# Kernel optimization log

Measured on AMD Instinct MI355X. Metric: run time of the kernel, lower is better.

Reference implementation:

```python
import jax, jax.numpy as jnp
import numpy as np

B, L, Q, H = 8192, 200, 128, 128

def setup_inputs() -> dict:
    key = jax.random.key(0)
    k1, k2, k3, k4 = jax.random.split(key, 4)
    query_ad = jax.random.normal(k1, (B, Q), dtype=jnp.float32)
    hist_behavior = jax.random.normal(k2, (B, L, H), dtype=jnp.float32)
    hist_behavior_length = jax.random.randint(k3, (B,), 0, L, dtype=jnp.int64)
    # xavier_normal for [Q, H] weight: std = sqrt(2/(Q+H))
    std = float(np.sqrt(2.0 / (Q + H)))
    biInt_weight = jax.random.normal(k4, (Q, H), dtype=jnp.float32) * std
    return {
        "query_ad": query_ad,
        "hist_behavior": hist_behavior,
        "hist_behavior_length": hist_behavior_length,
        "biInt_weight": biInt_weight,
    }

def reference(query_ad, hist_behavior, hist_behavior_length, biInt_weight):
    # bilinear attention logits: [B, L]
    logits = jnp.einsum('bq,qh,blh->bl', query_ad, biInt_weight, hist_behavior)
    # faithful to original: mask fills positions where arange < length with 1e-9
    L_ = hist_behavior.shape[1]
    mask = jnp.arange(L_)[None, :] < hist_behavior_length[:, None]  # [B, L]
    logits = jnp.where(mask, jnp.float32(1e-9), logits)
    score = jax.nn.softmax(logits, axis=-1)  # [B, L]
    out = jnp.einsum('bl,blh->bh', score, hist_behavior)  # [B, H]
    return out
```

## Files before the change

kernel.cpp:

```cpp
#include <hip/hip_runtime.h>
#include <math.h>

#define L_SEQ 200
#define Q_DIM 128
#define H_DIM 128

__global__ __launch_bounds__(256, 3) void attn_pool(
    const float* __restrict__ query,
    const float* __restrict__ hist,
    const int*   __restrict__ lens,
    const float* __restrict__ W,
    float* __restrict__ out)
{
    const int b = blockIdx.x;
    const int t = threadIdx.x;
    const int lane32 = t & 31;
    const int lgroup = t >> 5;
    const int wid    = t >> 6;

    __shared__ float s_q[Q_DIM];
    __shared__ float s_qw[H_DIM];
    __shared__ float s_part[8 * H_DIM];
    __shared__ float s_logits[L_SEQ];
    __shared__ float s_red[4];
    __shared__ float s_scalar[2];

    if (t < Q_DIM) s_q[t] = query[(size_t)b * Q_DIM + t];
    __syncthreads();
    {
        const int h  = t & 127;
        const int qh = t >> 7;
        float acc = 0.f;
        #pragma unroll 8
        for (int i = 0; i < 64; ++i) {
            const int q = qh * 64 + i;
            acc = fmaf(s_q[q], W[q * H_DIM + h], acc);
        }
        s_part[t] = acc;
    }
    __syncthreads();
    if (t < H_DIM) s_qw[t] = s_part[t] + s_part[t + 128];
    __syncthreads();

    const float4 qw4 = reinterpret_cast<const float4*>(s_qw)[lane32];

    const float* hrow = hist + (size_t)b * (L_SEQ * H_DIM);
    float4 r[25];
    #pragma unroll
    for (int i = 0; i < 25; ++i) {
        const int l = i * 8 + lgroup;
        r[i] = reinterpret_cast<const float4*>(hrow + l * H_DIM)[lane32];
    }

    #pragma unroll
    for (int i = 0; i < 25; ++i) {
        float p = qw4.x * r[i].x + qw4.y * r[i].y + qw4.z * r[i].z + qw4.w * r[i].w;
        p += __shfl_down(p, 16, 32);
        p += __shfl_down(p, 8, 32);
        p += __shfl_down(p, 4, 32);
        p += __shfl_down(p, 2, 32);
        p += __shfl_down(p, 1, 32);
        if (lane32 == 0) s_logits[i * 8 + lgroup] = p;
    }
    __syncthreads();

    const int len = lens[b];
    float x = -3.0e38f;
    if (t < L_SEQ) {
        const float v = s_logits[t];
        x = (t < len) ? 1e-9f : v;
    }
    float m = x;
    m = fmaxf(m, __shfl_down(m, 32));
    m = fmaxf(m, __shfl_down(m, 16));
    m = fmaxf(m, __shfl_down(m, 8));
    m = fmaxf(m, __shfl_down(m, 4));
    m = fmaxf(m, __shfl_down(m, 2));
    m = fmaxf(m, __shfl_down(m, 1));
    if ((t & 63) == 0) s_red[wid] = m;
    __syncthreads();
    if (t == 0)
        s_scalar[0] = fmaxf(fmaxf(s_red[0], s_red[1]), fmaxf(s_red[2], s_red[3]));
    __syncthreads();
    const float gmax = s_scalar[0];

    float e = 0.f;
    if (t < L_SEQ) {
        e = __expf(x - gmax);
        s_logits[t] = e;
    }
    float ssum = e;
    ssum += __shfl_down(ssum, 32);
    ssum += __shfl_down(ssum, 16);
    ssum += __shfl_down(ssum, 8);
    ssum += __shfl_down(ssum, 4);
    ssum += __shfl_down(ssum, 2);
    ssum += __shfl_down(ssum, 1);
    if ((t & 63) == 0) s_red[wid] = ssum;
    __syncthreads();
    if (t == 0) s_scalar[1] = s_red[0] + s_red[1] + s_red[2] + s_red[3];
    __syncthreads();
    const float inv = 1.0f / s_scalar[1];

    float4 acc = make_float4(0.f, 0.f, 0.f, 0.f);
    #pragma unroll
    for (int i = 0; i < 25; ++i) {
        const float s = s_logits[i * 8 + lgroup] * inv;
        acc.x = fmaf(s, r[i].x, acc.x);
        acc.y = fmaf(s, r[i].y, acc.y);
        acc.z = fmaf(s, r[i].z, acc.z);
        acc.w = fmaf(s, r[i].w, acc.w);
    }
    reinterpret_cast<float4*>(s_part)[lgroup * 32 + lane32] = acc;
    __syncthreads();
    if (t < H_DIM) {
        float v = 0.f;
        #pragma unroll
        for (int g = 0; g < 8; ++g) v += s_part[g * H_DIM + t];
        out[(size_t)b * H_DIM + t] = v;
    }
}

extern "C" void kernel_launch(void* const* d_in, const int* in_sizes, int n_in,
                              void* d_out, int out_size, void* d_ws, size_t ws_size,
                              hipStream_t stream) {
    const float* query = (const float*)d_in[0];
    const float* hist  = (const float*)d_in[1];
    const int*   lens  = (const int*)d_in[2];
    const float* W     = (const float*)d_in[3];
    float* out = (float*)d_out;

    const int B = in_sizes[2];
    attn_pool<<<dim3(B), dim3(256), 0, stream>>>(query, hist, lens, W, out);
}
```

Before: 1.040 ms.

## Split query-weight GEMV into batched kernel and widen attention pooling blocks

Moves the per-row q·W product into a separate kernel that handles eight batch rows per block and reuses each W load across them, writing the result to workspace (or to the output buffer when workspace is too small). The attention kernel now runs 512 threads per block with 13 registers of float4 history per thread. It skips logit dot products for masked positions and replaces the block-level softmax reductions with per-wavefront shuffle reductions, recomputing the exponentials in the pooling loop. The cost is an extra launch and an extra round trip of qw through global memory.

```diff
diff --git a/kernel.cpp b/kernel.cpp
--- a/kernel.cpp
+++ b/kernel.cpp
@@ -4,119 +4,152 @@
 #define L_SEQ 200
 #define Q_DIM 128
 #define H_DIM 128
+#define QBATCH 8
 
-__global__ __launch_bounds__(256, 3) void attn_pool(
+__global__ __launch_bounds__(256, 4) void qw_gemv(
     const float* __restrict__ query,
-    const float* __restrict__ hist,
-    const int*   __restrict__ lens,
     const float* __restrict__ W,
-    float* __restrict__ out)
+    float* __restrict__ qw)
 {
-    const int b = blockIdx.x;
-    const int t = threadIdx.x;
-    const int lane32 = t & 31;
-    const int lgroup = t >> 5;
-    const int wid    = t >> 6;
+    const int t    = threadIdx.x;
+    const int h    = t & 127;
+    const int half = t >> 7;
+    const int b0   = blockIdx.x * QBATCH;
 
-    __shared__ float s_q[Q_DIM];
-    __shared__ float s_qw[H_DIM];
-    __shared__ float s_part[8 * H_DIM];
-    __shared__ float s_logits[L_SEQ];
-    __shared__ float s_red[4];
-    __shared__ float s_scalar[2];
+    __shared__ float s_q[QBATCH][Q_DIM];
+    __shared__ float s_acc[2][QBATCH][H_DIM];
 
-    if (t < Q_DIM) s_q[t] = query[(size_t)b * Q_DIM + t];
-    __syncthreads();
     {
-        const int h  = t & 127;
-        const int qh = t >> 7;
-        float acc = 0.f;
-        #pragma unroll 8
-        for (int i = 0; i < 64; ++i) {
-            const int q = qh * 64 + i;
-            acc = fmaf(s_q[q], W[q * H_DIM + h], acc);
-        }
-        s_part[t] = acc;
-    }
-    __syncthreads();
-    if (t < H_DIM) s_qw[t] = s_part[t] + s_part[t + 128];
-    __syncthreads();
-
-    const float4 qw4 = reinterpret_cast<const float4*>(s_qw)[lane32];
-
-    const float* hrow = hist + (size_t)b * (L_SEQ * H_DIM);
-    float4 r[25];
-    #pragma unroll
-    for (int i = 0; i < 25; ++i) {
-        const int l = i * 8 + lgroup;
-        r[i] = reinterpret_cast<const float4*>(hrow + l * H_DIM)[lane32];
-    }
-
-    #pragma unroll
-    for (int i = 0; i < 25; ++i) {
-        float p = qw4.x * r[i].x + qw4.y * r[i].y + qw4.z * r[i].z + qw4.w * r[i].w;
-        p += __shfl_down(p, 16, 32);
-        p += __shfl_down(p, 8, 32);
-        p += __shfl_down(p, 4, 32);
-        p += __shfl_down(p, 2, 32);
-        p += __shfl_down(p, 1, 32);
-        if (lane32 == 0) s_logits[i * 8 + lgroup] = p;
+        const int bb = t >> 5;
+        const int f4 = t & 31;
+        reinterpret_cast<float4*>(&s_q[bb][0])[f4] =
+            reinterpret_cast<const float4*>(query + (size_t)(b0 + bb) * Q_DIM)[f4];
     }
     __syncthreads();
 
+    float acc[QBATCH] = {};
+    const float* Wcol = W + half * 64 * H_DIM + h;
+    #pragma unroll 4
+    for (int i = 0; i < 64; ++i) {
+        const float wq = Wcol[i * H_DIM];
+        const int   q  = half * 64 + i;
+        #pragma unroll
+        for (int bb = 0; bb < QBATCH; ++bb)
+            acc[bb] = fmaf(s_q[bb][q], wq, acc[bb]);
+    }
+    #pragma unroll
+    for (int bb = 0; bb < QBATCH; ++bb) s_acc[half][bb][h] = acc[bb];
+    __syncthreads();
+
+    #pragma unroll
+    for (int k = 0; k < 4; ++k) {
+        const int idx = k * 256 + t;
+        const int bb  = idx >> 7;
+        const int hh  = idx & 127;
+        qw[(size_t)(b0 + bb) * H_DIM + hh] = s_acc[0][bb][hh] + s_acc[1][bb][hh];
+    }
+}
+
+__global__ __launch_bounds__(512, 4) void attn_pool(
+    const float* qw_all,
+    const float* __restrict__ hist,
+    const int*   __restrict__ lens,
+    float*       out)
+{
+    const int b      = blockIdx.x;
+    const int t      = threadIdx.x;
+    const int lane32 = t & 31;
+    const int lane64 = t & 63;
+    const int lgroup = t >> 5;
+
+    __shared__ float s_logits[L_SEQ];
+    __shared__ float s_part[16 * H_DIM];
+
+    const float4* hbase =
+        reinterpret_cast<const float4*>(hist + (size_t)b * (L_SEQ * H_DIM));
+    float4 r[13];
+    #pragma unroll
+    for (int i = 0; i < 13; ++i) {
+        const int l = i * 16 + lgroup;
+        if (i < 12 || lgroup < 8)
+            r[i] = hbase[l * 32 + lane32];
+    }
+
+    const float4 qw4 =
+        reinterpret_cast<const float4*>(qw_all + (size_t)b * H_DIM)[lane32];
     const int len = lens[b];
-    float x = -3.0e38f;
-    if (t < L_SEQ) {
-        const float v = s_logits[t];
-        x = (t < len) ? 1e-9f : v;
+
+    #pragma unroll
+    for (int i = 0; i < 13; ++i) {
+        const int l = i * 16 + lgroup;
+        if (i < 12 || lgroup < 8) {
+            if (l >= len) {
+                float p = qw4.x * r[i].x + qw4.y * r[i].y
+                        + qw4.z * r[i].z + qw4.w * r[i].w;
+                p += __shfl_down(p, 16, 32);
+                p += __shfl_down(p,  8, 32);
+                p += __shfl_down(p,  4, 32);
+                p += __shfl_down(p,  2, 32);
+                p += __shfl_down(p,  1, 32);
+                if (lane32 == 0) s_logits[l] = p;
+            }
+        }
     }
-    float m = x;
-    m = fmaxf(m, __shfl_down(m, 32));
-    m = fmaxf(m, __shfl_down(m, 16));
-    m = fmaxf(m, __shfl_down(m, 8));
-    m = fmaxf(m, __shfl_down(m, 4));
-    m = fmaxf(m, __shfl_down(m, 2));
-    m = fmaxf(m, __shfl_down(m, 1));
-    if ((t & 63) == 0) s_red[wid] = m;
     __syncthreads();
-    if (t == 0)
-        s_scalar[0] = fmaxf(fmaxf(s_red[0], s_red[1]), fmaxf(s_red[2], s_red[3]));
-    __syncthreads();
-    const float gmax = s_scalar[0];
 
-    float e = 0.f;
-    if (t < L_SEQ) {
-        e = __expf(x - gmax);
-        s_logits[t] = e;
+    float xs[4];
+    float m = -3.0e38f;
+    #pragma unroll
+    for (int k = 0; k < 4; ++k) {
+        const int l = lane64 + k * 64;
+        float x = -3.0e38f;
+        if (l < L_SEQ) {
+            const float v = s_logits[l];
+            x = (l < len) ? 1e-9f : v;
+        }
+        xs[k] = x;
+        m = fmaxf(m, x);
     }
-    float ssum = e;
-    ssum += __shfl_down(ssum, 32);
-    ssum += __shfl_down(ssum, 16);
-    ssum += __shfl_down(ssum, 8);
-    ssum += __shfl_down(ssum, 4);
-    ssum += __shfl_down(ssum, 2);
-    ssum += __shfl_down(ssum, 1);
-    if ((t & 63) == 0) s_red[wid] = ssum;
-    __syncthreads();
-    if (t == 0) s_scalar[1] = s_red[0] + s_red[1] + s_red[2] + s_red[3];
-    __syncthreads();
-    const float inv = 1.0f / s_scalar[1];
+    m = fmaxf(m, __shfl_xor(m, 32, 64));
+    m = fmaxf(m, __shfl_xor(m, 16, 64));
+    m = fmaxf(m, __shfl_xor(m,  8, 64));
+    m = fmaxf(m, __shfl_xor(m,  4, 64));
+    m = fmaxf(m, __shfl_xor(m,  2, 64));
+    m = fmaxf(m, __shfl_xor(m,  1, 64));
+
+    float Z = 0.f;
+    #pragma unroll
+    for (int k = 0; k < 4; ++k)
+        Z += __expf(xs[k] - m);
+    Z += __shfl_xor(Z, 32, 64);
+    Z += __shfl_xor(Z, 16, 64);
+    Z += __shfl_xor(Z,  8, 64);
+    Z += __shfl_xor(Z,  4, 64);
+    Z += __shfl_xor(Z,  2, 64);
+    Z += __shfl_xor(Z,  1, 64);
+    const float inv = 1.0f / Z;
 
     float4 acc = make_float4(0.f, 0.f, 0.f, 0.f);
     #pragma unroll
-    for (int i = 0; i < 25; ++i) {
-        const float s = s_logits[i * 8 + lgroup] * inv;
-        acc.x = fmaf(s, r[i].x, acc.x);
-        acc.y = fmaf(s, r[i].y, acc.y);
-        acc.z = fmaf(s, r[i].z, acc.z);
-        acc.w = fmaf(s, r[i].w, acc.w);
+    for (int i = 0; i < 13; ++i) {
+        const int l = i * 16 + lgroup;
+        if (i < 12 || lgroup < 8) {
+            const float v = s_logits[l];
+            const float x = (l < len) ? 1e-9f : v;
+            const float s = __expf(x - m) * inv;
+            acc.x = fmaf(s, r[i].x, acc.x);
+            acc.y = fmaf(s, r[i].y, acc.y);
+            acc.z = fmaf(s, r[i].z, acc.z);
+            acc.w = fmaf(s, r[i].w, acc.w);
+        }
     }
     reinterpret_cast<float4*>(s_part)[lgroup * 32 + lane32] = acc;
     __syncthreads();
+
     if (t < H_DIM) {
         float v = 0.f;
         #pragma unroll
-        for (int g = 0; g < 8; ++g) v += s_part[g * H_DIM + t];
+        for (int g = 0; g < 16; ++g) v += s_part[g * H_DIM + t];
         out[(size_t)b * H_DIM + t] = v;
     }
 }
@@ -131,5 +164,10 @@
     float* out = (float*)d_out;
 
     const int B = in_sizes[2];
-    attn_pool<<<dim3(B), dim3(256), 0, stream>>>(query, hist, lens, W, out);
+
+    float* qwbuf = (d_ws != nullptr && ws_size >= (size_t)B * H_DIM * sizeof(float))
+                       ? (float*)d_ws : out;
+
+    qw_gemv<<<dim3(B / QBATCH), dim3(256), 0, stream>>>(query, W, qwbuf);
+    attn_pool<<<dim3(B), dim3(512), 0, stream>>>(qwbuf, hist, lens, out);
 }
```

New measurement: 1.050 ms. About the same (+0.9%).
